# Performance work log

Hardware: AMD Instinct MI355X
Metric: run time of the kernel (lower is better)

Reference implementation:

```python
import jax, jax.numpy as jnp
import numpy as np


def setup_inputs() -> dict:
    key = jax.random.key(0)
    ks = jax.random.split(key, 8)
    N, E, IN, ED, P, OUT = 50000, 400000, 128, 16, 3, 128
    return {
        "x": jax.random.normal(ks[0], (N, IN), dtype=jnp.float32),
        "edge_index": jax.random.randint(ks[1], (2, E), 0, N, dtype=jnp.int64),
        "edge_attr": jax.random.normal(ks[2], (E, ED), dtype=jnp.float32),
        "edge_time": jax.random.uniform(ks[3], (E,), dtype=jnp.float32),
        "current_time": jnp.ones((), dtype=jnp.float32),
        "W": jax.random.normal(ks[4], (P, IN + ED, OUT), dtype=jnp.float32) / np.sqrt(IN + ED),
        "b": jax.random.normal(ks[5], (P, OUT), dtype=jnp.float32) * 0.01,
        "decay": jnp.ones((P,), dtype=jnp.float32),
    }


def reference(x, edge_index, edge_attr, edge_time, current_time, W, b, decay):
    # x: [N, in_dim]; edge_index: [2, E]; edge_attr: [E, edge_dim]
    N = x.shape[0]
    src, dst = edge_index[0], edge_index[1]
    combined = jnp.concatenate([x[src], edge_attr], axis=-1)        # [E, in+edge]
    messages = jnp.einsum('ef,pfo->epo', combined, W) + b[None]     # [E, P, out]
    time_delta = current_time - edge_time                           # [E]
    temporal_weight = jnp.exp(-decay[None, :] * time_delta[:, None])  # [E, P]
    weighted = messages * temporal_weight[:, :, None]               # [E, P, out]
    # scatter-add per destination node -> [N, P, out]
    return jax.ops.segment_sum(weighted, dst, num_segments=N)
```

## Files before the change

kernel.cpp:

```cpp
#include <hip/hip_runtime.h>
#include <stdint.h>

#define N_NODES 50000
#define E_EDGES 400000
#define IN_DIM  128
#define ED_DIM  16
#define K_DIM   144
#define KT_N    5
#define P_N     3
#define OUT_DIM 128
#define NCOL    384
#define NT_N    24
#define ETILE   64
#define NBLK    6250
#define ASTRIDE 168

#define NC_PAD  50176
#define SB      196

typedef float  f32x4  __attribute__((ext_vector_type(4)));
typedef __bf16 bf16x8 __attribute__((ext_vector_type(8)));

__device__ __forceinline__ unsigned short f2bf(float f) {
    union { float f; unsigned u; } v; v.f = f;
    unsigned u = v.u + 0x7fffu + ((v.u >> 16) & 1u);
    return (unsigned short)(u >> 16);
}

__global__ void pack_w(const float* __restrict__ W, unsigned short* __restrict__ Bpack) {
    int idx = blockIdx.x * blockDim.x + threadIdx.x;
    if (idx >= NT_N * KT_N * 64 * 8) return;
    int j    = idx & 7;
    int lane = (idx >> 3) & 63;
    int kt   = (idx >> 9) % KT_N;
    int nt   = idx / (KT_N * 512);
    int nc   = lane & 15;
    int kr   = ((lane >> 4) << 3) + j;
    int f    = kt * 32 + kr;
    int n    = nt * 16 + nc;
    int p    = n >> 7;
    int o    = n & 127;
    float val = (f < K_DIM) ? W[(p * K_DIM + f) * OUT_DIM + o] : 0.0f;
    Bpack[idx] = f2bf(val);
}

__global__ void k_hist(const int* __restrict__ ei, int* __restrict__ counts) {
    int e = blockIdx.x * 256 + threadIdx.x;
    if (e < E_EDGES) atomicAdd(&counts[ei[E_EDGES + e]], 1);
}

__global__ void k_scan1(const int* __restrict__ counts, int* __restrict__ offsets,
                        int* __restrict__ bsums) {
    __shared__ int tmp[256];
    int t = threadIdx.x;
    int i = blockIdx.x * 256 + t;
    int v = counts[i];
    tmp[t] = v; __syncthreads();
    for (int off = 1; off < 256; off <<= 1) {
        int add = (t >= off) ? tmp[t - off] : 0;
        __syncthreads();
        tmp[t] += add;
        __syncthreads();
    }
    offsets[i] = tmp[t] - v;
    if (t == 255) bsums[blockIdx.x] = tmp[t];
}

__global__ void k_scan2(int* __restrict__ bsums) {
    __shared__ int tmp[256];
    int t = threadIdx.x;
    int v = (t < SB) ? bsums[t] : 0;
    tmp[t] = v; __syncthreads();
    for (int off = 1; off < 256; off <<= 1) {
        int add = (t >= off) ? tmp[t - off] : 0;
        __syncthreads();
        tmp[t] += add;
        __syncthreads();
    }
    if (t < SB) bsums[t] = tmp[t] - v;
}

__global__ void k_scan3(int* __restrict__ offsets, const int* __restrict__ bsums,
                        int* __restrict__ cursor) {
    int i = blockIdx.x * 256 + threadIdx.x;
    int v = offsets[i] + bsums[i >> 8];
    offsets[i] = v;
    cursor[i]  = v;
}

__global__ void k_scatter(const int* __restrict__ ei, const float* __restrict__ etime,
                          int* __restrict__ cursor, int4* __restrict__ equad) {
    int e = blockIdx.x * 256 + threadIdx.x;
    if (e >= E_EDGES) return;
    int d = ei[E_EDGES + e];
    int pos = atomicAdd(&cursor[d], 1);
    int4 q;
    q.x = ei[e];
    q.y = e;
    q.z = d;
    q.w = __float_as_int(etime[e]);
    equad[pos] = q;
}

__global__ __launch_bounds__(512) void mpc_phaseB(
    const float* __restrict__ x,
    const float* __restrict__ edge_attr,
    const float* __restrict__ current_time,
    const unsigned short* __restrict__ Bpack,
    const float* __restrict__ bvec,
    const float* __restrict__ decay,
    const int4*  __restrict__ equad,
    float* __restrict__ out)
{
    __shared__ __align__(16) unsigned short Alds[ETILE][ASTRIDE];
    __shared__ int   src_lds[ETILE];
    __shared__ int   pe_lds[ETILE];
    __shared__ int   dst_lds[ETILE];
    __shared__ float wt_lds[ETILE][P_N];

    const int tid = threadIdx.x;
    const int e0  = blockIdx.x * ETILE;
    const float ct = current_time[0];

    if (tid < ETILE) {
        int4 q = equad[e0 + tid];
        src_lds[tid] = q.x;
        pe_lds[tid]  = q.y;
        dst_lds[tid] = q.z;
        float dtv = ct - __int_as_float(q.w);
        wt_lds[tid][0] = __expf(-decay[0] * dtv);
        wt_lds[tid][1] = __expf(-decay[1] * dtv);
        wt_lds[tid][2] = __expf(-decay[2] * dtv);
    }
    __syncthreads();

    const float4* x4  = (const float4*)x;
    const float4* ea4 = (const float4*)edge_attr;
    for (int i = tid; i < ETILE * 40; i += 512) {
        int e = i / 40, q = i % 40;
        int se = (((e >> 2) & 3) << 4) | (((e >> 4) & 3) << 2) | (e & 3);
        uint2 val;
        if (q < 36) {
            float4 v;
            if (q < 32) v = x4[(size_t)src_lds[se] * 32 + q];
            else        v = ea4[(size_t)pe_lds[se] * 4 + (q - 32)];
            unsigned lo = (unsigned)f2bf(v.x) | ((unsigned)f2bf(v.y) << 16);
            unsigned hi = (unsigned)f2bf(v.z) | ((unsigned)f2bf(v.w) << 16);
            val = make_uint2(lo, hi);
        } else {
            val = make_uint2(0u, 0u);
        }
        *(uint2*)&Alds[e][q * 4] = val;
    }
    __syncthreads();

    const int w    = tid >> 6;
    const int lane = tid & 63;
    const int row  = lane & 15;
    const int khi  = lane >> 4;

    f32x4 acc[4][3];
#pragma unroll
    for (int mi = 0; mi < 4; ++mi)
#pragma unroll
        for (int ni = 0; ni < 3; ++ni)
            acc[mi][ni] = (f32x4){0.f, 0.f, 0.f, 0.f};

#pragma unroll
    for (int kt = 0; kt < KT_N; ++kt) {
        bf16x8 a[4], bf[3];
#pragma unroll
        for (int mi = 0; mi < 4; ++mi)
            a[mi] = *(const bf16x8*)&Alds[mi * 16 + row][kt * 32 + khi * 8];
#pragma unroll
        for (int ni = 0; ni < 3; ++ni) {
            int nt = w * 3 + ni;
            bf[ni] = *(const bf16x8*)&Bpack[(size_t)(((nt * KT_N) + kt) * 64 + lane) * 8];
        }
#pragma unroll
        for (int mi = 0; mi < 4; ++mi)
#pragma unroll
            for (int ni = 0; ni < 3; ++ni)
                acc[mi][ni] = __builtin_amdgcn_mfma_f32_16x16x32_bf16(
                    a[mi], bf[ni], acc[mi][ni], 0, 0, 0);
    }

    int   ncol[3], pcol[3];
    float bval[3];
#pragma unroll
    for (int ni = 0; ni < 3; ++ni) {
        ncol[ni] = (w * 3 + ni) * 16 + row;
        pcol[ni] = ncol[ni] >> 7;
        bval[ni] = bvec[ncol[ni]];
    }

    const int sbase = khi * 16;
    int dsp[16];
#pragma unroll
    for (int t = 0; t < 16; ++t) dsp[t] = dst_lds[sbase + t];

#pragma unroll
    for (int ni = 0; ni < 3; ++ni) {
        const int n = ncol[ni], p = pcol[ni];
        const float bv = bval[ni];
        float run = 0.0f;
        int   rd  = dsp[0];
#pragma unroll
        for (int t = 0; t < 16; ++t) {
            float c = (acc[t >> 2][ni][t & 3] + bv) * wt_lds[sbase + t][p];
            int d = dsp[t];
            if (d != rd) {
                atomicAdd(&out[(size_t)rd * NCOL + n], run);
                run = 0.0f;
                rd  = d;
            }
            run += c;
        }
        atomicAdd(&out[(size_t)rd * NCOL + n], run);
    }
}

extern "C" void kernel_launch(void* const* d_in, const int* in_sizes, int n_in,
                              void* d_out, int out_size, void* d_ws, size_t ws_size,
                              hipStream_t stream) {
    const float* x            = (const float*)d_in[0];
    const int*   edge_index   = (const int*)d_in[1];
    const float* edge_attr    = (const float*)d_in[2];
    const float* edge_time    = (const float*)d_in[3];
    const float* current_time = (const float*)d_in[4];
    const float* W            = (const float*)d_in[5];
    const float* bvec         = (const float*)d_in[6];
    const float* decay        = (const float*)d_in[7];
    float* out = (float*)d_out;

    char* ws = (char*)d_ws;
    unsigned short* Bpack = (unsigned short*)(ws);
    int*   counts  = (int*)  (ws + 122880);
    int*   offsets = (int*)  (ws + 323584);
    int*   cursor  = (int*)  (ws + 524288);
    int*   bsums   = (int*)  (ws + 724992);
    int4*  equad   = (int4*) (ws + 726016);

    hipMemsetAsync(counts, 0, (size_t)NC_PAD * 4, stream);
    hipMemsetAsync(d_out, 0, (size_t)out_size * sizeof(float), stream);

    pack_w<<<(NT_N * KT_N * 64 * 8 + 255) / 256, 256, 0, stream>>>(W, Bpack);

    k_hist   <<<(E_EDGES + 255) / 256, 256, 0, stream>>>(edge_index, counts);
    k_scan1  <<<SB, 256, 0, stream>>>(counts, offsets, bsums);
    k_scan2  <<<1, 256, 0, stream>>>(bsums);
    k_scan3  <<<SB, 256, 0, stream>>>(offsets, bsums, cursor);
    k_scatter<<<(E_EDGES + 255) / 256, 256, 0, stream>>>(edge_index, edge_time, cursor, equad);

    mpc_phaseB<<<NBLK, 512, 0, stream>>>(x, edge_attr, current_time, Bpack, bvec,
                                         decay, equad, out);
}
```

Before: 332.4 us.

## Merge three scan kernels into one and use plain stores for interior segments

Replaces the three-kernel exclusive scan over destination counts with a single 1024-thread block, where each thread handles 49 consecutive counts. This removes two kernel launches and the offsets/bsums buffers. In the main kernel, a destination run that is fully contained within a lane's 16-edge slice is now written with a plain store instead of an atomicAdd. Atomics are kept only for runs that may continue into neighbouring slices or blocks, which are detected by reading the adjacent destinations. The single-block scan serializes roughly 50K elements on one CU, and the chunked reads in it are strided and uncoalesced.

```diff
diff --git a/kernel.cpp b/kernel.cpp
--- a/kernel.cpp
+++ b/kernel.cpp
@@ -16,7 +16,8 @@
 #define ASTRIDE 168
 
 #define NC_PAD  50176
-#define SB      196
+#define SCAN_T  1024
+#define SCAN_C  49
 
 typedef float  f32x4  __attribute__((ext_vector_type(4)));
 typedef __bf16 bf16x8 __attribute__((ext_vector_type(8)));
@@ -49,43 +50,27 @@
     if (e < E_EDGES) atomicAdd(&counts[ei[E_EDGES + e]], 1);
 }
 
-__global__ void k_scan1(const int* __restrict__ counts, int* __restrict__ offsets,
-                        int* __restrict__ bsums) {
-    __shared__ int tmp[256];
-    int t = threadIdx.x;
-    int i = blockIdx.x * 256 + t;
-    int v = counts[i];
-    tmp[t] = v; __syncthreads();
-    for (int off = 1; off < 256; off <<= 1) {
-        int add = (t >= off) ? tmp[t - off] : 0;
+__global__ __launch_bounds__(SCAN_T) void k_scan(const int* __restrict__ counts,
+                                                 int* __restrict__ cursor) {
+    __shared__ int tsum[SCAN_T];
+    const int t = threadIdx.x;
+    const int base = t * SCAN_C;
+    int s = 0;
+    for (int i = 0; i < SCAN_C; ++i) s += counts[base + i];
+    tsum[t] = s;
+    __syncthreads();
+    for (int off = 1; off < SCAN_T; off <<= 1) {
+        int add = (t >= off) ? tsum[t - off] : 0;
         __syncthreads();
-        tmp[t] += add;
+        tsum[t] += add;
         __syncthreads();
     }
-    offsets[i] = tmp[t] - v;
-    if (t == 255) bsums[blockIdx.x] = tmp[t];
-}
-
-__global__ void k_scan2(int* __restrict__ bsums) {
-    __shared__ int tmp[256];
-    int t = threadIdx.x;
-    int v = (t < SB) ? bsums[t] : 0;
-    tmp[t] = v; __syncthreads();
-    for (int off = 1; off < 256; off <<= 1) {
-        int add = (t >= off) ? tmp[t - off] : 0;
-        __syncthreads();
-        tmp[t] += add;
-        __syncthreads();
-    }
-    if (t < SB) bsums[t] = tmp[t] - v;
-}
-
-__global__ void k_scan3(int* __restrict__ offsets, const int* __restrict__ bsums,
-                        int* __restrict__ cursor) {
-    int i = blockIdx.x * 256 + threadIdx.x;
-    int v = offsets[i] + bsums[i >> 8];
-    offsets[i] = v;
-    cursor[i]  = v;
+    int run = tsum[t] - s;
+    for (int i = 0; i < SCAN_C; ++i) {
+        int c = counts[base + i];
+        cursor[base + i] = run;
+        run += c;
+    }
 }
 
 __global__ void k_scatter(const int* __restrict__ ei, const float* __restrict__ etime,
@@ -117,6 +102,7 @@
     __shared__ int   pe_lds[ETILE];
     __shared__ int   dst_lds[ETILE];
     __shared__ float wt_lds[ETILE][P_N];
+    __shared__ int   pn_dst[2];
 
     const int tid = threadIdx.x;
     const int e0  = blockIdx.x * ETILE;
@@ -131,6 +117,10 @@
         wt_lds[tid][0] = __expf(-decay[0] * dtv);
         wt_lds[tid][1] = __expf(-decay[1] * dtv);
         wt_lds[tid][2] = __expf(-decay[2] * dtv);
+    } else if (tid == ETILE) {
+        const int* ez = (const int*)equad;
+        pn_dst[0] = (e0 > 0) ? ez[(size_t)(e0 - 1) * 4 + 2] : -1;
+        pn_dst[1] = (e0 + ETILE < E_EDGES) ? ez[(size_t)(e0 + ETILE) * 4 + 2] : -1;
     }
     __syncthreads();
 
@@ -198,6 +188,8 @@
     int dsp[16];
 #pragma unroll
     for (int t = 0; t < 16; ++t) dsp[t] = dst_lds[sbase + t];
+    const int prev_dst = (khi > 0) ? dst_lds[sbase - 1]  : pn_dst[0];
+    const int next_dst = (khi < 3) ? dst_lds[sbase + 16] : pn_dst[1];
 
 #pragma unroll
     for (int ni = 0; ni < 3; ++ni) {
@@ -205,18 +197,24 @@
         const float bv = bval[ni];
         float run = 0.0f;
         int   rd  = dsp[0];
+        bool  head = true;
 #pragma unroll
         for (int t = 0; t < 16; ++t) {
             float c = (acc[t >> 2][ni][t & 3] + bv) * wt_lds[sbase + t][p];
             int d = dsp[t];
             if (d != rd) {
-                atomicAdd(&out[(size_t)rd * NCOL + n], run);
+                float* dst = &out[(size_t)rd * NCOL + n];
+                if (head && rd == prev_dst) atomicAdd(dst, run);
+                else                        *dst = run;
+                head = false;
                 run = 0.0f;
                 rd  = d;
             }
             run += c;
         }
-        atomicAdd(&out[(size_t)rd * NCOL + n], run);
+        float* dst = &out[(size_t)rd * NCOL + n];
+        if ((head && rd == prev_dst) || rd == next_dst) atomicAdd(dst, run);
+        else                                            *dst = run;
     }
 }
 
@@ -236,10 +234,8 @@
     char* ws = (char*)d_ws;
     unsigned short* Bpack = (unsigned short*)(ws);
     int*   counts  = (int*)  (ws + 122880);
-    int*   offsets = (int*)  (ws + 323584);
-    int*   cursor  = (int*)  (ws + 524288);
-    int*   bsums   = (int*)  (ws + 724992);
-    int4*  equad   = (int4*) (ws + 726016);
+    int*   cursor  = (int*)  (ws + 323584);
+    int4*  equad   = (int4*) (ws + 524288);
 
     hipMemsetAsync(counts, 0, (size_t)NC_PAD * 4, stream);
     hipMemsetAsync(d_out, 0, (size_t)out_size * sizeof(float), stream);
@@ -247,9 +243,7 @@
     pack_w<<<(NT_N * KT_N * 64 * 8 + 255) / 256, 256, 0, stream>>>(W, Bpack);
 
     k_hist   <<<(E_EDGES + 255) / 256, 256, 0, stream>>>(edge_index, counts);
-    k_scan1  <<<SB, 256, 0, stream>>>(counts, offsets, bsums);
-    k_scan2  <<<1, 256, 0, stream>>>(bsums);
-    k_scan3  <<<SB, 256, 0, stream>>>(offsets, bsums, cursor);
+    k_scan   <<<1, SCAN_T, 0, stream>>>(counts, cursor);
     k_scatter<<<(E_EDGES + 255) / 256, 256, 0, stream>>>(edge_index, edge_time, cursor, equad);
 
     mpc_phaseB<<<NBLK, 512, 0, stream>>>(x, edge_attr, current_time, Bpack, bvec,
```

New measurement: 342.5 us. 3.0% more time.
